# Optimization experiments

Measured on AMD Instinct MI355X. Metric: run time of the kernel, lower is better.

The kernel has to match this reference:

```python
import jax, jax.numpy as jnp
import numpy as np

B, C, H, W = 4, 128, 64, 64
HEADS, DH, MEM = 4, 32, 16
HID = HEADS * DH  # 128


def setup_inputs() -> dict:
    key = jax.random.key(0)
    k1, k2, k3, k4, k5 = jax.random.split(key, 5)
    return {
        "x": jax.random.normal(k1, (B, C, H, W), jnp.float32),
        "memory": jax.random.normal(k2, (1, C, 1, MEM), jnp.float32),
        "w_qkv": jax.random.normal(k3, (3 * HID, C), jnp.float32) * 0.05,  # conv1x1, bias=False
        "w_out": jax.random.normal(k4, (C, HID), jnp.float32) * 0.05,      # conv1x1 weight
        "b_out": jax.random.normal(k5, (C,), jnp.float32) * 0.01,          # conv1x1 bias
    }


def reference(x, memory, w_qkv, w_out, b_out):
    b, c, h, w = x.shape
    hw = h * w
    scale = DH ** -0.5

    # flatten spatial, append memory tokens along token axis
    x_flat = x.reshape(b, c, hw)                         # (b, c, hw)
    mem = jnp.broadcast_to(memory[:, :, 0, :], (b, c, MEM))
    x_ext = jnp.concatenate([x_flat, mem], axis=2)       # (b, c, n) n = hw + MEM

    # 1x1 conv QKV projection == channel matmul
    qkv = jnp.einsum('oc,bcn->bon', w_qkv, x_ext)        # (b, 3*HID, n)
    q, k, v = jnp.split(qkv, 3, axis=1)                  # each (b, HID, n)

    def to_heads(t):
        return t.reshape(b, HEADS, DH, -1)               # (b, h, d, n)

    q = to_heads(q) * scale
    k = to_heads(k)
    v = to_heads(v)

    sim = jnp.einsum('bhdi,bhdj->bhij', q, k)            # (b, h, n, n)
    attn = jax.nn.softmax(sim, axis=-1)                  # stable softmax (amax-sub inside)
    out = jnp.einsum('bhij,bhdj->bhid', attn, v)         # (b, h, n, d)

    out = out[:, :, :hw]                                 # drop memory-token queries
    out = out.transpose(0, 1, 3, 2).reshape(b, HID, h, w)  # b (h d) x y

    return jnp.einsum('oc,bchw->bohw', w_out, out) + b_out[None, :, None, None]
```

## Files before the change

kernel.cpp:

```cpp
#include <hip/hip_runtime.h>
#include <hip/hip_bf16.h>

constexpr int NQ   = 4096;
constexpr int NKV  = 4112;
constexpr int NP   = 4160;
constexpr int CDIM = 128;
constexpr int NSL  = 2;
constexpr float QSC = 0.17677669529663687f * 1.4426950408889634f;

typedef __attribute__((ext_vector_type(8)))  short bf16x8;
typedef __attribute__((ext_vector_type(4)))  short bf16x4;
typedef __attribute__((ext_vector_type(4)))  float f32x4;
typedef __attribute__((ext_vector_type(16))) float f32x16;

static __device__ __forceinline__ unsigned short bfbits(float f) {
  __hip_bfloat16 h = __float2bfloat16(f);
  return *reinterpret_cast<unsigned short*>(&h);
}
static __device__ __forceinline__ unsigned pk2(float a, float b) {
  return (unsigned)bfbits(a) | ((unsigned)bfbits(b) << 16);
}

__global__ __launch_bounds__(256) void k1_qkv(
    const float* __restrict__ x, const float* __restrict__ memry,
    const float* __restrict__ wqkv, const float* __restrict__ wout,
    __hip_bfloat16* __restrict__ Qt, __hip_bfloat16* __restrict__ Kt,
    __hip_bfloat16* __restrict__ Vt, __hip_bfloat16* __restrict__ Wb) {
  __shared__ __align__(16) __hip_bfloat16 xt[64][136];
  const int b  = blockIdx.y;
  const int nb = blockIdx.x * 64;
  const int t  = threadIdx.x;
  const int wv = t >> 6, ln = t & 63;

  if (blockIdx.x == 0 && b == 0) {
    for (int i = t; i < CDIM * CDIM; i += 256) Wb[i] = __float2bfloat16(wout[i]);
  }

  {
    const int n = nb + ln;
    #pragma unroll
    for (int i = 0; i < 16; ++i) {
      const int c = wv * 32 + 2 * i;
      float v0 = 0.f, v1 = 0.f;
      if (n < NQ)        { v0 = x[((size_t)b * CDIM + c) * NQ + n];
                           v1 = x[((size_t)b * CDIM + c + 1) * NQ + n]; }
      else if (n < NKV)  { v0 = memry[c * 16 + (n - NQ)];
                           v1 = memry[(c + 1) * 16 + (n - NQ)]; }
      *reinterpret_cast<unsigned*>(&xt[ln][c]) =
          (unsigned)bfbits(v0) | ((unsigned)bfbits(v1) << 16);
    }
  }
  __syncthreads();

  const int li = ln & 15, g = ln >> 4;
  bf16x8 xa[4][4];
  #pragma unroll
  for (int nt = 0; nt < 4; ++nt)
    #pragma unroll
    for (int k = 0; k < 4; ++k)
      xa[nt][k] = *reinterpret_cast<const bf16x8*>(&xt[nt * 16 + li][k * 32 + 8 * g]);

  #pragma unroll
  for (int oi = 0; oi < 6; ++oi) {
    const int ot = wv * 6 + oi;
    bf16x8 wf[4];
    #pragma unroll
    for (int k = 0; k < 4; ++k) {
      const float* wp = &wqkv[(size_t)(ot * 16 + li) * CDIM + k * 32 + 8 * g];
      const float4 f0 = *reinterpret_cast<const float4*>(wp);
      const float4 f1 = *reinterpret_cast<const float4*>(wp + 4);
      bf16x8 wc;
      wc[0] = (short)bfbits(f0.x); wc[1] = (short)bfbits(f0.y);
      wc[2] = (short)bfbits(f0.z); wc[3] = (short)bfbits(f0.w);
      wc[4] = (short)bfbits(f1.x); wc[5] = (short)bfbits(f1.y);
      wc[6] = (short)bfbits(f1.z); wc[7] = (short)bfbits(f1.w);
      wf[k] = wc;
    }
    #pragma unroll
    for (int nt = 0; nt < 4; ++nt) {
      f32x4 a; a[0] = a[1] = a[2] = a[3] = 0.f;
      if (ot < 16) {
        #pragma unroll
        for (int k = 0; k < 4; ++k)
          a = __builtin_amdgcn_mfma_f32_16x16x32_bf16(xa[nt][k], wf[k], a, 0, 0, 0);
        const int o = ot * 16 + li;
        const int h = (o >> 5) & 3, d = o & 31;
        if (ot < 8) {
          #pragma unroll
          for (int r = 0; r < 4; ++r) {
            const int n = nb + nt * 16 + 4 * g + r;
            Qt[((size_t)(b * 4 + h) * NP + n) * 32 + d] = __float2bfloat16(a[r] * QSC);
          }
        } else {
          #pragma unroll
          for (int r = 0; r < 4; ++r) {
            const int n = nb + nt * 16 + 4 * g + r;
            Kt[((size_t)(b * 4 + h) * NP + n) * 32 + d] = __float2bfloat16(a[r]);
          }
        }
      } else {
        #pragma unroll
        for (int k = 0; k < 4; ++k)
          a = __builtin_amdgcn_mfma_f32_16x16x32_bf16(wf[k], xa[nt][k], a, 0, 0, 0);
        #pragma unroll
        for (int r = 0; r < 4; ++r) {
          const int o = ot * 16 + 4 * g + r;
          const int h = (o >> 5) & 3, d = o & 31;
          const int n = nb + nt * 16 + li;
          Vt[((size_t)(b * 4 + h) * 32 + d) * NP + n] = __float2bfloat16(a[r]);
        }
      }
    }
  }
}


#if __has_builtin(__builtin_amdgcn_mfma_f32_32x32x8bf16_1k)
#define HAS_PV8 1
#else
#define HAS_PV8 0
#endif

__global__ __launch_bounds__(256, 4) void k2_attn(
    const __hip_bfloat16* __restrict__ Qt, const __hip_bfloat16* __restrict__ Kt,
    const __hip_bfloat16* __restrict__ Vt, float* __restrict__ Pb,
    float* __restrict__ Lb) {
  __shared__ __align__(16) unsigned char smem[16384];

  const int wg  = blockIdx.x;
  const int xcd = wg & 7;
  const int i   = wg >> 3;
  const int bh  = 2 * xcd + (i & 1);
  const int sl  = (i >> 1) & 1;
  const int wv  = threadIdx.x >> 6, lane = threadIdx.x & 63;
  const int lq  = lane & 31, hi = lane >> 5;
  const int qb  = (i >> 2) * 128 + wv * 32;

  const bf16x8 qf0 = *reinterpret_cast<const bf16x8*>(
      Qt + ((size_t)bh * NP + qb + lq) * 32 + 8 * hi);
  const bf16x8 qf1 = *reinterpret_cast<const bf16x8*>(
      Qt + ((size_t)bh * NP + qb + lq) * 32 + 16 + 8 * hi);

  const int kb0 = sl * 2048;
  const __hip_bfloat16* Ksrc = Kt + ((size_t)bh * NP + kb0 + (wv >> 1) * 32 + lq) * 32
                                  + (wv & 1) * 16 + 8 * hi;
  const __hip_bfloat16* Vsrc = Vt + ((size_t)bh * 32 + lq) * NP + kb0 + wv * 16 + 8 * hi;
  const int dstoff = wv * 1024 + lane * 16;

  f32x16 acc0, acc1, z;
  #pragma unroll
  for (int q = 0; q < 16; ++q) { acc0[q] = 0.f; acc1[q] = 0.f; z[q] = 0.f; }
  float l0 = 0.f, l1 = 0.f, l2 = 0.f, l3 = 0.f;

  bf16x8 kreg = *reinterpret_cast<const bf16x8*>(Ksrc);
  bf16x8 vreg = *reinterpret_cast<const bf16x8*>(Vsrc);
  *reinterpret_cast<bf16x8*>(smem + dstoff)        = kreg;
  *reinterpret_cast<bf16x8*>(smem + 4096 + dstoff) = vreg;
  kreg = *reinterpret_cast<const bf16x8*>(Ksrc + 2048);
  vreg = *reinterpret_cast<const bf16x8*>(Vsrc + 64);

  for (int t = 0; t < 32; ++t) {
    __syncthreads();
    const int p = t & 1;
    if (t < 31) {
      unsigned char* nb = smem + (p ^ 1) * 8192;
      *reinterpret_cast<bf16x8*>(nb + dstoff)        = kreg;
      *reinterpret_cast<bf16x8*>(nb + 4096 + dstoff) = vreg;
      if (t < 30) {
        kreg = *reinterpret_cast<const bf16x8*>(Ksrc + (size_t)(t + 2) * 2048);
        vreg = *reinterpret_cast<const bf16x8*>(Vsrc + (t + 2) * 64);
      }
    }
    const __hip_bfloat16* kbuf = (const __hip_bfloat16*)(smem + p * 8192);
    const __hip_bfloat16* vbuf = (const __hip_bfloat16*)(smem + p * 8192 + 4096);

    #pragma unroll
    for (int st = 0; st < 2; ++st) {
      const bf16x8 kf0 = *reinterpret_cast<const bf16x8*>(kbuf + st * 1024 + lane * 8);
      const bf16x8 kf1 = *reinterpret_cast<const bf16x8*>(kbuf + st * 1024 + 512 + lane * 8);
      f32x16 s = __builtin_amdgcn_mfma_f32_32x32x16_bf16(kf0, qf0, z, 0, 0, 0);
      s = __builtin_amdgcn_mfma_f32_32x32x16_bf16(kf1, qf1, s, 0, 0, 0);
      float p_[16];
      #pragma unroll
      for (int r = 0; r < 16; ++r) p_[r] = __builtin_amdgcn_exp2f(s[r]);
      l0 += (p_[0] + p_[1]) + (p_[2] + p_[3]);
      l1 += (p_[4] + p_[5]) + (p_[6] + p_[7]);
      l2 += (p_[8] + p_[9]) + (p_[10] + p_[11]);
      l3 += (p_[12] + p_[13]) + (p_[14] + p_[15]);
#if HAS_PV8
      union UU { unsigned u[2]; bf16x4 v; };
      UU a0, a1, a2, a3;
      a0.u[0] = pk2(p_[0], p_[1]);   a0.u[1] = pk2(p_[2], p_[3]);
      a1.u[0] = pk2(p_[4], p_[5]);   a1.u[1] = pk2(p_[6], p_[7]);
      a2.u[0] = pk2(p_[8], p_[9]);   a2.u[1] = pk2(p_[10], p_[11]);
      a3.u[0] = pk2(p_[12], p_[13]); a3.u[1] = pk2(p_[14], p_[15]);
      const __hip_bfloat16* vb = vbuf + st * 1024 + lq * 8 + hi * 4;
      const bf16x4 vf0 = *reinterpret_cast<const bf16x4*>(vb);
      const bf16x4 vf1 = *reinterpret_cast<const bf16x4*>(vb + 256);
      const bf16x4 vf2 = *reinterpret_cast<const bf16x4*>(vb + 512);
      const bf16x4 vf3 = *reinterpret_cast<const bf16x4*>(vb + 768);
      acc0 = __builtin_amdgcn_mfma_f32_32x32x8bf16_1k(a0.v, vf0, acc0, 0, 0, 0);
      acc0 = __builtin_amdgcn_mfma_f32_32x32x8bf16_1k(a1.v, vf1, acc0, 0, 0, 0);
      acc1 = __builtin_amdgcn_mfma_f32_32x32x8bf16_1k(a2.v, vf2, acc1, 0, 0, 0);
      acc1 = __builtin_amdgcn_mfma_f32_32x32x8bf16_1k(a3.v, vf3, acc1, 0, 0, 0);
#else
      unsigned a0u0 = pk2(p_[0], p_[1]),   a0u1 = pk2(p_[2], p_[3]);
      unsigned a1u0 = pk2(p_[4], p_[5]),   a1u1 = pk2(p_[6], p_[7]);
      unsigned a2u0 = pk2(p_[8], p_[9]),   a2u1 = pk2(p_[10], p_[11]);
      unsigned a3u0 = pk2(p_[12], p_[13]), a3u1 = pk2(p_[14], p_[15]);
      union U8 { unsigned u[4]; bf16x8 v; };
      const bf16x8 vh0 = *reinterpret_cast<const bf16x8*>(vbuf + (2 * st) * 512 + lane * 8);
      const bf16x8 vh1 = *reinterpret_cast<const bf16x8*>(vbuf + (2 * st + 1) * 512 + lane * 8);
      {
        const unsigned s0 = __shfl_xor(hi ? a0u0 : a1u0, 32, 64);
        const unsigned s1 = __shfl_xor(hi ? a0u1 : a1u1, 32, 64);
        U8 f;
        f.u[0] = hi ? s0 : a0u0; f.u[1] = hi ? s1 : a0u1;
        f.u[2] = hi ? a1u0 : s0; f.u[3] = hi ? a1u1 : s1;
        acc0 = __builtin_amdgcn_mfma_f32_32x32x16_bf16(f.v, vh0, acc0, 0, 0, 0);
      }
      {
        const unsigned s0 = __shfl_xor(hi ? a2u0 : a3u0, 32, 64);
        const unsigned s1 = __shfl_xor(hi ? a2u1 : a3u1, 32, 64);
        U8 f;
        f.u[0] = hi ? s0 : a2u0; f.u[1] = hi ? s1 : a2u1;
        f.u[2] = hi ? a3u0 : s0; f.u[3] = hi ? a3u1 : s1;
        acc1 = __builtin_amdgcn_mfma_f32_32x32x16_bf16(f.v, vh1, acc1, 0, 0, 0);
      }
#endif
    }
  }

  if (sl == NSL - 1) {
    const __hip_bfloat16* Kp   = Kt + (size_t)bh * NP * 32 + (size_t)lq * 32 + 8 * hi;
    const __hip_bfloat16* Vrow = Vt + ((size_t)bh * 32 + lq) * NP;
    const int kb = 4096;
    const bf16x8 kf0 = *reinterpret_cast<const bf16x8*>(Kp + (size_t)kb * 32);
    const bf16x8 kf1 = *reinterpret_cast<const bf16x8*>(Kp + (size_t)kb * 32 + 16);
    f32x16 s = __builtin_amdgcn_mfma_f32_32x32x16_bf16(kf0, qf0, z, 0, 0, 0);
    s = __builtin_amdgcn_mfma_f32_32x32x16_bf16(kf1, qf1, s, 0, 0, 0);
    float p_[8];
    #pragma unroll
    for (int r = 0; r < 8; ++r) p_[r] = __builtin_amdgcn_exp2f(s[r]);
    l0 += (p_[0] + p_[1]) + (p_[2] + p_[3]);
    l1 += (p_[4] + p_[5]) + (p_[6] + p_[7]);
#if HAS_PV8
    union UU { unsigned u[2]; bf16x4 v; };
    UU a0, a1;
    a0.u[0] = pk2(p_[0], p_[1]); a0.u[1] = pk2(p_[2], p_[3]);
    a1.u[0] = pk2(p_[4], p_[5]); a1.u[1] = pk2(p_[6], p_[7]);
    const bf16x4 vf0 = *reinterpret_cast<const bf16x4*>(Vrow + kb + 4 * hi);
    const bf16x4 vf1 = *reinterpret_cast<const bf16x4*>(Vrow + kb + 8 + 4 * hi);
    acc0 = __builtin_amdgcn_mfma_f32_32x32x8bf16_1k(a0.v, vf0, acc0, 0, 0, 0);
    acc0 = __builtin_amdgcn_mfma_f32_32x32x8bf16_1k(a1.v, vf1, acc0, 0, 0, 0);
#else
    unsigned a0u0 = pk2(p_[0], p_[1]), a0u1 = pk2(p_[2], p_[3]);
    unsigned a1u0 = pk2(p_[4], p_[5]), a1u1 = pk2(p_[6], p_[7]);
    union U8 { unsigned u[4]; bf16x8 v; };
    const unsigned s0 = __shfl_xor(hi ? a0u0 : a1u0, 32, 64);
    const unsigned s1 = __shfl_xor(hi ? a0u1 : a1u1, 32, 64);
    U8 f;
    f.u[0] = hi ? s0 : a0u0; f.u[1] = hi ? s1 : a0u1;
    f.u[2] = hi ? a1u0 : s0; f.u[3] = hi ? a1u1 : s1;
    const bf16x8 vf = *reinterpret_cast<const bf16x8*>(Vrow + kb + 8 * hi);
    acc0 = __builtin_amdgcn_mfma_f32_32x32x16_bf16(f.v, vf, acc0, 0, 0, 0);
#endif
  }

  float* Pp = Pb + (((size_t)sl * 16 + bh) * NQ + qb) * 32;
  #pragma unroll
  for (int r = 0; r < 16; ++r) {
    const int q = (r & 3) + 8 * (r >> 2) + 4 * hi;
    Pp[(size_t)q * 32 + lq] = acc0[r] + acc1[r];
  }
  float lsum = (l0 + l1) + (l2 + l3);
  lsum += __shfl_xor(lsum, 32, 64);
  if (hi == 0)
    Lb[((size_t)sl * 16 + bh) * NQ + qb + lq] = lsum;
}

__global__ __launch_bounds__(256) void k2b_combine(
    const float* __restrict__ Pb, const float* __restrict__ Lb,
    __hip_bfloat16* __restrict__ att) {
  const int idx = blockIdx.x * 256 + threadIdx.x;
  const int bh = idx >> 12;
  const int q  = idx & 4095;
  constexpr size_t PS = (size_t)16 * NQ * 32;
  constexpr size_t LS = (size_t)16 * NQ;
  const float* p = Pb + ((size_t)bh * NQ + q) * 32;

  float l = 0.f;
  #pragma unroll
  for (int s = 0; s < NSL; ++s) l += Lb[s * LS + (size_t)bh * NQ + q];
  const float inv = 1.f / l;

  float o[32];
  #pragma unroll
  for (int j = 0; j < 8; ++j) {
    const float4 f = *reinterpret_cast<const float4*>(p + 4 * j);
    o[4*j] = f.x; o[4*j+1] = f.y; o[4*j+2] = f.z; o[4*j+3] = f.w;
  }
  #pragma unroll
  for (int s = 1; s < NSL; ++s)
    #pragma unroll
    for (int j = 0; j < 8; ++j) {
      const float4 f = *reinterpret_cast<const float4*>(p + s * PS + 4 * j);
      o[4*j] += f.x; o[4*j+1] += f.y; o[4*j+2] += f.z; o[4*j+3] += f.w;
    }

  unsigned wb[16];
  #pragma unroll
  for (int j = 0; j < 16; ++j) wb[j] = pk2(o[2*j] * inv, o[2*j+1] * inv);
  __hip_bfloat16* dst = att + ((size_t)bh * NQ + q) * 32;
  *reinterpret_cast<uint4*>(dst)      = make_uint4(wb[0],  wb[1],  wb[2],  wb[3]);
  *reinterpret_cast<uint4*>(dst + 8)  = make_uint4(wb[4],  wb[5],  wb[6],  wb[7]);
  *reinterpret_cast<uint4*>(dst + 16) = make_uint4(wb[8],  wb[9],  wb[10], wb[11]);
  *reinterpret_cast<uint4*>(dst + 24) = make_uint4(wb[12], wb[13], wb[14], wb[15]);
}

__global__ __launch_bounds__(256) void k3_proj(
    const __hip_bfloat16* __restrict__ att, const __hip_bfloat16* __restrict__ Wb,
    const float* __restrict__ bout, float* __restrict__ out) {
  const int b = blockIdx.y, nb = blockIdx.x * 64;
  const int wv = threadIdx.x >> 6, lane = threadIdx.x & 63;
  const int li = lane & 15, g = lane >> 4;

  bf16x8 wf[2][4];
  float bo[2][4];
  #pragma unroll
  for (int tt = 0; tt < 2; ++tt) {
    const int ot = 2 * wv + tt;
    #pragma unroll
    for (int k = 0; k < 4; ++k)
      wf[tt][k] = *reinterpret_cast<const bf16x8*>(
          &Wb[(size_t)(ot * 16 + li) * CDIM + k * 32 + 8 * g]);
    #pragma unroll
    for (int r = 0; r < 4; ++r) bo[tt][r] = bout[ot * 16 + 4 * g + r];
  }
  #pragma unroll
  for (int nt = 0; nt < 4; ++nt) {
    bf16x8 bfr[4];
    #pragma unroll
    for (int k = 0; k < 4; ++k)
      bfr[k] = *reinterpret_cast<const bf16x8*>(
          &att[(((size_t)(b * 4 + k)) * NQ + nb + nt * 16 + li) * 32 + 8 * g]);
    #pragma unroll
    for (int tt = 0; tt < 2; ++tt) {
      f32x4 a; a[0] = a[1] = a[2] = a[3] = 0.f;
      #pragma unroll
      for (int k = 0; k < 4; ++k)
        a = __builtin_amdgcn_mfma_f32_16x16x32_bf16(wf[tt][k], bfr[k], a, 0, 0, 0);
      const int ot = 2 * wv + tt;
      #pragma unroll
      for (int r = 0; r < 4; ++r)
        out[((size_t)b * CDIM + ot * 16 + 4 * g + r) * NQ + nb + nt * 16 + li] =
            a[r] + bo[tt][r];
    }
  }
}

extern "C" void kernel_launch(void* const* d_in, const int* in_sizes, int n_in,
                              void* d_out, int out_size, void* d_ws, size_t ws_size,
                              hipStream_t stream) {
  const float* x    = (const float*)d_in[0];
  const float* memp = (const float*)d_in[1];
  const float* wqkv = (const float*)d_in[2];
  const float* wout = (const float*)d_in[3];
  const float* bout = (const float*)d_in[4];
  float* out = (float*)d_out;

  char* ws = (char*)d_ws;
  const size_t SZ  = (size_t)16 * NP * 32 * 2;
  const size_t PSZ = (size_t)NSL * 16 * NQ * 32 * 4;
  const size_t LSZ = (size_t)NSL * 16 * NQ * 4;
  const size_t ASZ = (size_t)16 * NQ * 32 * 2;
  __hip_bfloat16* Qt  = (__hip_bfloat16*)(ws);
  __hip_bfloat16* Kt  = (__hip_bfloat16*)(ws + SZ);
  __hip_bfloat16* Vt  = (__hip_bfloat16*)(ws + 2 * SZ);
  float*          Pbf = (float*)(ws + 3 * SZ);
  float*          Lbf = (float*)(ws + 3 * SZ + PSZ);
  __hip_bfloat16* att = (__hip_bfloat16*)(ws + 3 * SZ + PSZ + LSZ);
  __hip_bfloat16* Wb  = (__hip_bfloat16*)(ws + 3 * SZ + PSZ + LSZ + ASZ);

  hipLaunchKernelGGL(k1_qkv, dim3(65, 4), dim3(256), 0, stream,
                     x, memp, wqkv, wout, Qt, Kt, Vt, Wb);
  hipLaunchKernelGGL(k2_attn, dim3(1024), dim3(256), 0, stream,
                     Qt, Kt, Vt, Pbf, Lbf);
  hipLaunchKernelGGL(k2b_combine, dim3(256), dim3(256), 0, stream, Pbf, Lbf, att);
  hipLaunchKernelGGL(k3_proj, dim3(64, 4), dim3(256), 0, stream, att, Wb, bout, out);
}
```

Baseline: 98.04 us.

## Raise split-KV factor to four and widen grids across all kernels

The attention kernel now splits each head's key range into four slices instead of two, doubling its grid and halving its loop length. The QKV projection kernel is split along a new z grid dimension over output tiles, and the projection kernel processes half as many tokens per block. The combine kernel is remapped so each thread handles four output dims of one query, with XCD-aware block mapping for coalesced loads. The aim is more blocks in flight and shorter per-block latency on every stage, at the cost of twice as much partial-sum traffic and more reduction work in the combine step.

```diff
diff --git a/kernel.cpp b/kernel.cpp
--- a/kernel.cpp
+++ b/kernel.cpp
@@ -5,7 +5,7 @@
 constexpr int NKV  = 4112;
 constexpr int NP   = 4160;
 constexpr int CDIM = 128;
-constexpr int NSL  = 2;
+constexpr int NSL  = 4;
 constexpr float QSC = 0.17677669529663687f * 1.4426950408889634f;
 
 typedef __attribute__((ext_vector_type(8)))  short bf16x8;
@@ -28,11 +28,12 @@
     __hip_bfloat16* __restrict__ Vt, __hip_bfloat16* __restrict__ Wb) {
   __shared__ __align__(16) __hip_bfloat16 xt[64][136];
   const int b  = blockIdx.y;
+  const int zz = blockIdx.z;
   const int nb = blockIdx.x * 64;
   const int t  = threadIdx.x;
   const int wv = t >> 6, ln = t & 63;
 
-  if (blockIdx.x == 0 && b == 0) {
+  if (blockIdx.x == 0 && b == 0 && zz == 0) {
     for (int i = t; i < CDIM * CDIM; i += 256) Wb[i] = __float2bfloat16(wout[i]);
   }
 
@@ -61,8 +62,8 @@
       xa[nt][k] = *reinterpret_cast<const bf16x8*>(&xt[nt * 16 + li][k * 32 + 8 * g]);
 
   #pragma unroll
-  for (int oi = 0; oi < 6; ++oi) {
-    const int ot = wv * 6 + oi;
+  for (int oi = 0; oi < 3; ++oi) {
+    const int ot = zz * 12 + wv * 3 + oi;
     bf16x8 wf[4];
     #pragma unroll
     for (int k = 0; k < 4; ++k) {
@@ -131,17 +132,17 @@
   const int xcd = wg & 7;
   const int i   = wg >> 3;
   const int bh  = 2 * xcd + (i & 1);
-  const int sl  = (i >> 1) & 1;
+  const int sl  = (i >> 1) & 3;
   const int wv  = threadIdx.x >> 6, lane = threadIdx.x & 63;
   const int lq  = lane & 31, hi = lane >> 5;
-  const int qb  = (i >> 2) * 128 + wv * 32;
+  const int qb  = (i >> 3) * 128 + wv * 32;
 
   const bf16x8 qf0 = *reinterpret_cast<const bf16x8*>(
       Qt + ((size_t)bh * NP + qb + lq) * 32 + 8 * hi);
   const bf16x8 qf1 = *reinterpret_cast<const bf16x8*>(
       Qt + ((size_t)bh * NP + qb + lq) * 32 + 16 + 8 * hi);
 
-  const int kb0 = sl * 2048;
+  const int kb0 = sl * 1024;
   const __hip_bfloat16* Ksrc = Kt + ((size_t)bh * NP + kb0 + (wv >> 1) * 32 + lq) * 32
                                   + (wv & 1) * 16 + 8 * hi;
   const __hip_bfloat16* Vsrc = Vt + ((size_t)bh * 32 + lq) * NP + kb0 + wv * 16 + 8 * hi;
@@ -159,14 +160,14 @@
   kreg = *reinterpret_cast<const bf16x8*>(Ksrc + 2048);
   vreg = *reinterpret_cast<const bf16x8*>(Vsrc + 64);
 
-  for (int t = 0; t < 32; ++t) {
+  for (int t = 0; t < 16; ++t) {
     __syncthreads();
     const int p = t & 1;
-    if (t < 31) {
-      unsigned char* nb = smem + (p ^ 1) * 8192;
-      *reinterpret_cast<bf16x8*>(nb + dstoff)        = kreg;
-      *reinterpret_cast<bf16x8*>(nb + 4096 + dstoff) = vreg;
-      if (t < 30) {
+    if (t < 15) {
+      unsigned char* nbuf = smem + (p ^ 1) * 8192;
+      *reinterpret_cast<bf16x8*>(nbuf + dstoff)        = kreg;
+      *reinterpret_cast<bf16x8*>(nbuf + 4096 + dstoff) = vreg;
+      if (t < 14) {
         kreg = *reinterpret_cast<const bf16x8*>(Ksrc + (size_t)(t + 2) * 2048);
         vreg = *reinterpret_cast<const bf16x8*>(Vsrc + (t + 2) * 64);
       }
@@ -282,46 +283,37 @@
 __global__ __launch_bounds__(256) void k2b_combine(
     const float* __restrict__ Pb, const float* __restrict__ Lb,
     __hip_bfloat16* __restrict__ att) {
-  const int idx = blockIdx.x * 256 + threadIdx.x;
-  const int bh = idx >> 12;
-  const int q  = idx & 4095;
   constexpr size_t PS = (size_t)16 * NQ * 32;
   constexpr size_t LS = (size_t)16 * NQ;
-  const float* p = Pb + ((size_t)bh * NQ + q) * 32;
+  const int wg  = blockIdx.x;
+  const int xcd = wg & 7;
+  const int i   = wg >> 3;
+  const int bh  = 2 * xcd + (i & 1);
+  const int j   = i >> 1;
+  const int u   = j * 256 + threadIdx.x;
+  const int q   = u >> 3;
+  const int d0  = (u & 7) * 4;
+  const size_t qi = (size_t)bh * NQ + q;
 
   float l = 0.f;
   #pragma unroll
-  for (int s = 0; s < NSL; ++s) l += Lb[s * LS + (size_t)bh * NQ + q];
+  for (int s = 0; s < NSL; ++s) l += Lb[s * LS + qi];
   const float inv = 1.f / l;
 
-  float o[32];
-  #pragma unroll
-  for (int j = 0; j < 8; ++j) {
-    const float4 f = *reinterpret_cast<const float4*>(p + 4 * j);
-    o[4*j] = f.x; o[4*j+1] = f.y; o[4*j+2] = f.z; o[4*j+3] = f.w;
-  }
-  #pragma unroll
-  for (int s = 1; s < NSL; ++s)
-    #pragma unroll
-    for (int j = 0; j < 8; ++j) {
-      const float4 f = *reinterpret_cast<const float4*>(p + s * PS + 4 * j);
-      o[4*j] += f.x; o[4*j+1] += f.y; o[4*j+2] += f.z; o[4*j+3] += f.w;
-    }
-
-  unsigned wb[16];
-  #pragma unroll
-  for (int j = 0; j < 16; ++j) wb[j] = pk2(o[2*j] * inv, o[2*j+1] * inv);
-  __hip_bfloat16* dst = att + ((size_t)bh * NQ + q) * 32;
-  *reinterpret_cast<uint4*>(dst)      = make_uint4(wb[0],  wb[1],  wb[2],  wb[3]);
-  *reinterpret_cast<uint4*>(dst + 8)  = make_uint4(wb[4],  wb[5],  wb[6],  wb[7]);
-  *reinterpret_cast<uint4*>(dst + 16) = make_uint4(wb[8],  wb[9],  wb[10], wb[11]);
-  *reinterpret_cast<uint4*>(dst + 24) = make_uint4(wb[12], wb[13], wb[14], wb[15]);
+  float4 o = make_float4(0.f, 0.f, 0.f, 0.f);
+  #pragma unroll
+  for (int s = 0; s < NSL; ++s) {
+    const float4 f = *reinterpret_cast<const float4*>(Pb + s * PS + qi * 32 + d0);
+    o.x += f.x; o.y += f.y; o.z += f.z; o.w += f.w;
+  }
+  *reinterpret_cast<uint2*>(att + qi * 32 + d0) =
+      make_uint2(pk2(o.x * inv, o.y * inv), pk2(o.z * inv, o.w * inv));
 }
 
 __global__ __launch_bounds__(256) void k3_proj(
     const __hip_bfloat16* __restrict__ att, const __hip_bfloat16* __restrict__ Wb,
     const float* __restrict__ bout, float* __restrict__ out) {
-  const int b = blockIdx.y, nb = blockIdx.x * 64;
+  const int b = blockIdx.y, nb = blockIdx.x * 32;
   const int wv = threadIdx.x >> 6, lane = threadIdx.x & 63;
   const int li = lane & 15, g = lane >> 4;
 
@@ -338,7 +330,7 @@
     for (int r = 0; r < 4; ++r) bo[tt][r] = bout[ot * 16 + 4 * g + r];
   }
   #pragma unroll
-  for (int nt = 0; nt < 4; ++nt) {
+  for (int nt = 0; nt < 2; ++nt) {
     bf16x8 bfr[4];
     #pragma unroll
     for (int k = 0; k < 4; ++k)
@@ -382,10 +374,10 @@
   __hip_bfloat16* att = (__hip_bfloat16*)(ws + 3 * SZ + PSZ + LSZ);
   __hip_bfloat16* Wb  = (__hip_bfloat16*)(ws + 3 * SZ + PSZ + LSZ + ASZ);
 
-  hipLaunchKernelGGL(k1_qkv, dim3(65, 4), dim3(256), 0, stream,
+  hipLaunchKernelGGL(k1_qkv, dim3(65, 4, 2), dim3(256), 0, stream,
                      x, memp, wqkv, wout, Qt, Kt, Vt, Wb);
-  hipLaunchKernelGGL(k2_attn, dim3(1024), dim3(256), 0, stream,
+  hipLaunchKernelGGL(k2_attn, dim3(2048), dim3(256), 0, stream,
                      Qt, Kt, Vt, Pbf, Lbf);
-  hipLaunchKernelGGL(k2b_combine, dim3(256), dim3(256), 0, stream, Pbf, Lbf, att);
-  hipLaunchKernelGGL(k3_proj, dim3(64, 4), dim3(256), 0, stream, att, Wb, bout, out);
-}
+  hipLaunchKernelGGL(k2b_combine, dim3(2048), dim3(256), 0, stream, Pbf, Lbf, att);
+  hipLaunchKernelGGL(k3_proj, dim3(128, 4), dim3(256), 0, stream, att, Wb, bout, out);
+}
```

Result: faster. 94.62 us (-3.5%).
